# Kernel tuning notes

Hardware: AMD Instinct MI355X
Metric: run time of the kernel (lower is better)

The kernel has to match this reference:

```python
import jax, jax.numpy as jnp
import numpy as np

N_NODES = 10000
N_EDGES = 640000
D_FEAT = 128


def setup_inputs() -> dict:
    key = jax.random.key(0)
    k1, k2, k3 = jax.random.split(key, 3)
    node_feats = jax.random.normal(k1, (N_NODES, D_FEAT), dtype=jnp.float32)
    src = jax.random.randint(k2, (N_EDGES,), 0, N_NODES, dtype=jnp.int64)
    dst = jax.random.randint(k3, (N_EDGES,), 0, N_NODES, dtype=jnp.int64)
    return {"node_feats": node_feats, "src": src, "dst": dst}


def reference(node_feats, src, dst):
    # copy_u: message on each edge is the source node's feature -> [E, D]
    # max reduce: per-destination segment max -> [N, D]
    messages = node_feats[src]
    h_max = jax.ops.segment_max(messages, dst, num_segments=N_NODES)
    # DGL fills nodes with zero in-degree with 0 for max reduce; segment_max
    # yields -inf for empty segments, so replace those with 0.
    in_deg = jax.ops.segment_sum(
        jnp.ones((dst.shape[0],), dtype=jnp.int32), dst, num_segments=N_NODES
    )
    h_max = jnp.where((in_deg > 0)[:, None], h_max, jnp.zeros((), node_feats.dtype))
    return h_max
```

## Files before the change

kernel.cpp:

```cpp
#include <hip/hip_runtime.h>
#include <math.h>

#define NBINS   10000
#define NB      256
#define PSTRIDE 10016
#define HWORDS  5008
#define PAD     160

__device__ __forceinline__ unsigned short f2bf(float x) {
    unsigned int u = __float_as_uint(x);
    unsigned int r = (u + 0x7fffu + ((u >> 16) & 1u)) >> 16;
    return (unsigned short)r;
}
__device__ __forceinline__ float bf2f(unsigned short b) {
    return __uint_as_float(((unsigned int)b) << 16);
}

__global__ __launch_bounds__(256) void hist_convert_kernel(
        const int* __restrict__ dst, const float* __restrict__ feats,
        unsigned short* __restrict__ partial, unsigned short* __restrict__ feats_bf,
        int E, int chunk, int nf4) {
    const float4* f4 = (const float4*)feats;
    ushort4* b4 = (ushort4*)feats_bf;
    for (int i = blockIdx.x * blockDim.x + threadIdx.x; i < nf4;
         i += gridDim.x * blockDim.x) {
        float4 v = f4[i];
        ushort4 o;
        o.x = f2bf(v.x); o.y = f2bf(v.y); o.z = f2bf(v.z); o.w = f2bf(v.w);
        b4[i] = o;
    }
    __shared__ unsigned int h[HWORDS];
    for (int i = threadIdx.x; i < HWORDS; i += 256) h[i] = 0u;
    __syncthreads();
    int b = blockIdx.x;
    int start = b * chunk;
    int end   = min(start + chunk, E);
    for (int e = start + threadIdx.x; e < end; e += 256) {
        int d = dst[e];
        atomicAdd(&h[d >> 1], 1u << ((d & 1) * 16));
    }
    __syncthreads();
    unsigned int* row = (unsigned int*)(partial + (size_t)b * PSTRIDE);
    for (int i = threadIdx.x; i < HWORDS; i += 256) row[i] = h[i];
}

__global__ __launch_bounds__(256) void colscan_kernel(unsigned short* __restrict__ partial,
                                                      int* __restrict__ deg, int nbins) {
    int bin = blockIdx.x * blockDim.x + threadIdx.x;
    if (bin >= nbins) return;
    int running = 0;
    for (int b = 0; b < NB; b += 16) {
        int v[16];
        #pragma unroll
        for (int k = 0; k < 16; k++)
            v[k] = partial[(size_t)(b + k) * PSTRIDE + bin];
        #pragma unroll
        for (int k = 0; k < 16; k++) {
            partial[(size_t)(b + k) * PSTRIDE + bin] = (unsigned short)running;
            running += v[k];
        }
    }
    deg[bin] = running;
}

__global__ __launch_bounds__(256) void scatter_kernel(const int* __restrict__ src,
                                                      const int* __restrict__ dst,
                                                      const unsigned short* __restrict__ partial,
                                                      unsigned short* __restrict__ edge_pad,
                                                      int E, int chunk) {
    __shared__ unsigned int h[HWORDS];
    for (int i = threadIdx.x; i < HWORDS; i += 256) h[i] = 0u;
    __syncthreads();
    int b = blockIdx.x;
    const unsigned short* base = partial + (size_t)b * PSTRIDE;
    int start = b * chunk;
    int end   = min(start + chunk, E);
    for (int e = start + threadIdx.x; e < end; e += 256) {
        int d = dst[e];
        unsigned int old = atomicAdd(&h[d >> 1], 1u << ((d & 1) * 16));
        int r = (int)((old >> ((d & 1) * 16)) & 0xffffu);
        edge_pad[(size_t)d * PAD + (int)base[d] + r] = (unsigned short)src[e];
    }
}

__global__ __launch_bounds__(256) void gather_max_kernel(
        const unsigned short* __restrict__ feats_bf, const int* __restrict__ deg,
        const unsigned short* __restrict__ edge_pad, float* __restrict__ out,
        int n_nodes) {
    int gtid    = blockIdx.x * blockDim.x + threadIdx.x;
    int wave_id = gtid >> 6;
    int lane    = threadIdx.x & 63;
    int half    = lane >> 5;
    int col     = lane & 31;
    int node    = wave_id * 2 + half;
    if (node >= n_nodes) return;

    int dg = deg[node];
    const unsigned short* ep = edge_pad + (size_t)node * PAD;
    const ushort4* f4 = (const ushort4*)feats_bf;
    float4 acc = make_float4(-INFINITY, -INFINITY, -INFINITY, -INFINITY);

    int j = 0;
    for (; j + 8 <= dg; j += 8) {
        uint4 w = *(const uint4*)(ep + j);
        int e0 = w.x & 0xffff, e1 = w.x >> 16;
        int e2 = w.y & 0xffff, e3 = w.y >> 16;
        int e4 = w.z & 0xffff, e5 = w.z >> 16;
        int e6 = w.w & 0xffff, e7 = w.w >> 16;
        ushort4 v0 = f4[(size_t)e0 * 32 + col];
        ushort4 v1 = f4[(size_t)e1 * 32 + col];
        ushort4 v2 = f4[(size_t)e2 * 32 + col];
        ushort4 v3 = f4[(size_t)e3 * 32 + col];
        ushort4 v4 = f4[(size_t)e4 * 32 + col];
        ushort4 v5 = f4[(size_t)e5 * 32 + col];
        ushort4 v6 = f4[(size_t)e6 * 32 + col];
        ushort4 v7 = f4[(size_t)e7 * 32 + col];
        acc.x = fmaxf(acc.x, fmaxf(fmaxf(fmaxf(bf2f(v0.x), bf2f(v1.x)), fmaxf(bf2f(v2.x), bf2f(v3.x))),
                                   fmaxf(fmaxf(bf2f(v4.x), bf2f(v5.x)), fmaxf(bf2f(v6.x), bf2f(v7.x)))));
        acc.y = fmaxf(acc.y, fmaxf(fmaxf(fmaxf(bf2f(v0.y), bf2f(v1.y)), fmaxf(bf2f(v2.y), bf2f(v3.y))),
                                   fmaxf(fmaxf(bf2f(v4.y), bf2f(v5.y)), fmaxf(bf2f(v6.y), bf2f(v7.y)))));
        acc.z = fmaxf(acc.z, fmaxf(fmaxf(fmaxf(bf2f(v0.z), bf2f(v1.z)), fmaxf(bf2f(v2.z), bf2f(v3.z))),
                                   fmaxf(fmaxf(bf2f(v4.z), bf2f(v5.z)), fmaxf(bf2f(v6.z), bf2f(v7.z)))));
        acc.w = fmaxf(acc.w, fmaxf(fmaxf(fmaxf(bf2f(v0.w), bf2f(v1.w)), fmaxf(bf2f(v2.w), bf2f(v3.w))),
                                   fmaxf(fmaxf(bf2f(v4.w), bf2f(v5.w)), fmaxf(bf2f(v6.w), bf2f(v7.w)))));
    }
    for (; j < dg; ++j) {
        int e0 = ep[j];
        ushort4 v = f4[(size_t)e0 * 32 + col];
        acc.x = fmaxf(acc.x, bf2f(v.x));
        acc.y = fmaxf(acc.y, bf2f(v.y));
        acc.z = fmaxf(acc.z, bf2f(v.z));
        acc.w = fmaxf(acc.w, bf2f(v.w));
    }

    if (dg == 0) { acc.x = 0.f; acc.y = 0.f; acc.z = 0.f; acc.w = 0.f; }
    ((float4*)out)[(size_t)node * 32 + col] = acc;
}

extern "C" void kernel_launch(void* const* d_in, const int* in_sizes, int n_in,
                              void* d_out, int out_size, void* d_ws, size_t ws_size,
                              hipStream_t stream) {
    const float* feats = (const float*)d_in[0];
    const int*   src   = (const int*)d_in[1];
    const int*   dst   = (const int*)d_in[2];
    float*       out   = (float*)d_out;

    const int E = in_sizes[1];
    const int N = NBINS;
    const int chunk = (E + NB - 1) / NB;
    const int nf4   = (N * 128) / 4;

    char* w = (char*)d_ws;
    unsigned short* partial = (unsigned short*)w;
    w += (size_t)NB * PSTRIDE * sizeof(unsigned short);
    int* deg = (int*)w;  w += (size_t)PSTRIDE * sizeof(int);
    unsigned short* edge_pad = (unsigned short*)w;
    w += (size_t)N * PAD * sizeof(unsigned short);
    unsigned short* feats_bf = (unsigned short*)w;

    hist_convert_kernel<<<NB, 256, 0, stream>>>(dst, feats, partial, feats_bf, E, chunk, nf4);
    colscan_kernel<<<(N + 255) / 256, 256, 0, stream>>>(partial, deg, N);
    scatter_kernel<<<NB, 256, 0, stream>>>(src, dst, partial, edge_pad, E, chunk);

    int waves    = (N + 1) / 2;
    int threads  = waves * 64;
    int blocks_g = (threads + 255) / 256;
    gather_max_kernel<<<blocks_g, 256, 0, stream>>>(feats_bf, deg, edge_pad, out, N);
}
```

Measured before the change: 107.1 us.

## Fuse histogram, scan and scatter into one per-chunk local counting-sort kernel

Replaces the three-kernel global CSR build (per-block histograms, column scan, padded scatter) with a single kernel. Sixteen blocks each sort a 40000-edge chunk locally in shared memory and write per-node offsets into a small transposed table. The gather kernel then walks 16 segments per node instead of one contiguous padded list. This saves launches and the large partial-histogram traffic, but the gather now does more scattered index loads and serial per-segment loops, and only 16 blocks do the sort.

```diff
diff --git a/kernel.cpp b/kernel.cpp
--- a/kernel.cpp
+++ b/kernel.cpp
@@ -2,10 +2,10 @@
 #include <math.h>
 
 #define NBINS   10000
-#define NB      256
-#define PSTRIDE 10016
+#define NBS     16
+#define CHUNK   40000
 #define HWORDS  5008
-#define PAD     160
+#define TROW    16
 
 __device__ __forceinline__ unsigned short f2bf(float x) {
     unsigned int u = __float_as_uint(x);
@@ -16,77 +16,90 @@
     return __uint_as_float(((unsigned int)b) << 16);
 }
 
-__global__ __launch_bounds__(256) void hist_convert_kernel(
-        const int* __restrict__ dst, const float* __restrict__ feats,
-        unsigned short* __restrict__ partial, unsigned short* __restrict__ feats_bf,
-        int E, int chunk, int nf4) {
-    const float4* f4 = (const float4*)feats;
-    ushort4* b4 = (ushort4*)feats_bf;
-    for (int i = blockIdx.x * blockDim.x + threadIdx.x; i < nf4;
-         i += gridDim.x * blockDim.x) {
-        float4 v = f4[i];
-        ushort4 o;
-        o.x = f2bf(v.x); o.y = f2bf(v.y); o.z = f2bf(v.z); o.w = f2bf(v.w);
-        b4[i] = o;
+__global__ __launch_bounds__(256) void build_kernel(
+        const int* __restrict__ dst, const int* __restrict__ src,
+        const float* __restrict__ feats, unsigned short* __restrict__ trans,
+        unsigned short* __restrict__ edge_sorted, unsigned short* __restrict__ feats_bf,
+        int E, int nf4) {
+    {
+        const float4* f4 = (const float4*)feats;
+        ushort4* b4 = (ushort4*)feats_bf;
+        for (int i = blockIdx.x * blockDim.x + threadIdx.x; i < nf4;
+             i += gridDim.x * blockDim.x) {
+            float4 v = f4[i];
+            ushort4 o;
+            o.x = f2bf(v.x); o.y = f2bf(v.y); o.z = f2bf(v.z); o.w = f2bf(v.w);
+            b4[i] = o;
+        }
     }
+    if (blockIdx.x >= NBS) return;
+
     __shared__ unsigned int h[HWORDS];
-    for (int i = threadIdx.x; i < HWORDS; i += 256) h[i] = 0u;
+    __shared__ int wsums[4];
+    const int b   = blockIdx.x;
+    const int tid = threadIdx.x;
+    const int lane = tid & 63;
+    const int wave = tid >> 6;
+    const int start = b * CHUNK;
+    const int end   = min(start + CHUNK, E);
+
+    for (int i = tid; i < HWORDS; i += 256) h[i] = 0u;
     __syncthreads();
-    int b = blockIdx.x;
-    int start = b * chunk;
-    int end   = min(start + chunk, E);
-    for (int e = start + threadIdx.x; e < end; e += 256) {
+    for (int e = start + tid; e < end; e += 256) {
         int d = dst[e];
         atomicAdd(&h[d >> 1], 1u << ((d & 1) * 16));
     }
     __syncthreads();
-    unsigned int* row = (unsigned int*)(partial + (size_t)b * PSTRIDE);
-    for (int i = threadIdx.x; i < HWORDS; i += 256) row[i] = h[i];
-}
 
-__global__ __launch_bounds__(256) void colscan_kernel(unsigned short* __restrict__ partial,
-                                                      int* __restrict__ deg, int nbins) {
-    int bin = blockIdx.x * blockDim.x + threadIdx.x;
-    if (bin >= nbins) return;
-    int running = 0;
-    for (int b = 0; b < NB; b += 16) {
-        int v[16];
-        #pragma unroll
-        for (int k = 0; k < 16; k++)
-            v[k] = partial[(size_t)(b + k) * PSTRIDE + bin];
-        #pragma unroll
-        for (int k = 0; k < 16; k++) {
-            partial[(size_t)(b + k) * PSTRIDE + bin] = (unsigned short)running;
-            running += v[k];
-        }
+    int w0 = tid * 20;
+    int w1 = min(w0 + 20, HWORDS);
+    int s = 0;
+    for (int w = w0; w < w1; ++w) {
+        unsigned int u = h[w];
+        s += (int)(u & 0xffffu) + (int)(u >> 16);
     }
-    deg[bin] = running;
-}
+    int incl = s;
+    #pragma unroll
+    for (int off = 1; off < 64; off <<= 1) {
+        int t = __shfl_up(incl, off, 64);
+        if (lane >= off) incl += t;
+    }
+    if (lane == 63) wsums[wave] = incl;
+    __syncthreads();
+    int wpre = 0;
+    #pragma unroll
+    for (int k = 0; k < 4; k++) if (k < wave) wpre += wsums[k];
+    int running = wpre + incl - s;
+    for (int w = w0; w < w1; ++w) {
+        unsigned int u = h[w];
+        int c0 = (int)(u & 0xffffu);
+        int c1 = (int)(u >> 16);
+        h[w] = (unsigned int)running | ((unsigned int)(running + c0) << 16);
+        running += c0 + c1;
+    }
+    __syncthreads();
 
-__global__ __launch_bounds__(256) void scatter_kernel(const int* __restrict__ src,
-                                                      const int* __restrict__ dst,
-                                                      const unsigned short* __restrict__ partial,
-                                                      unsigned short* __restrict__ edge_pad,
-                                                      int E, int chunk) {
-    __shared__ unsigned int h[HWORDS];
-    for (int i = threadIdx.x; i < HWORDS; i += 256) h[i] = 0u;
+    for (int i = tid; i < NBINS; i += 256) {
+        unsigned int u = h[i >> 1];
+        trans[(size_t)i * TROW + b] = (unsigned short)((u >> ((i & 1) * 16)) & 0xffffu);
+    }
+    if (tid == 0) trans[(size_t)NBINS * TROW + b] = (unsigned short)max(0, end - start);
     __syncthreads();
-    int b = blockIdx.x;
-    const unsigned short* base = partial + (size_t)b * PSTRIDE;
-    int start = b * chunk;
-    int end   = min(start + chunk, E);
-    for (int e = start + threadIdx.x; e < end; e += 256) {
+
+    unsigned short* reg = edge_sorted + (size_t)b * CHUNK;
+    for (int e = start + tid; e < end; e += 256) {
         int d = dst[e];
         unsigned int old = atomicAdd(&h[d >> 1], 1u << ((d & 1) * 16));
-        int r = (int)((old >> ((d & 1) * 16)) & 0xffffu);
-        edge_pad[(size_t)d * PAD + (int)base[d] + r] = (unsigned short)src[e];
+        int pos = (int)((old >> ((d & 1) * 16)) & 0xffffu);
+        reg[pos] = (unsigned short)src[e];
     }
 }
 
 __global__ __launch_bounds__(256) void gather_max_kernel(
-        const unsigned short* __restrict__ feats_bf, const int* __restrict__ deg,
-        const unsigned short* __restrict__ edge_pad, float* __restrict__ out,
-        int n_nodes) {
+        const unsigned short* __restrict__ feats_bf,
+        const unsigned short* __restrict__ trans,
+        const unsigned short* __restrict__ edge_sorted,
+        float* __restrict__ out, int n_nodes) {
     int gtid    = blockIdx.x * blockDim.x + threadIdx.x;
     int wave_id = gtid >> 6;
     int lane    = threadIdx.x & 63;
@@ -95,45 +108,45 @@
     int node    = wave_id * 2 + half;
     if (node >= n_nodes) return;
 
-    int dg = deg[node];
-    const unsigned short* ep = edge_pad + (size_t)node * PAD;
+    const uint4* tp = (const uint4*)trans;
+    union { uint4 v[2]; unsigned short s[16]; } O0, O1;
+    O0.v[0] = tp[(size_t)node * 2];
+    O0.v[1] = tp[(size_t)node * 2 + 1];
+    O1.v[0] = tp[(size_t)(node + 1) * 2];
+    O1.v[1] = tp[(size_t)(node + 1) * 2 + 1];
+
     const ushort4* f4 = (const ushort4*)feats_bf;
     float4 acc = make_float4(-INFINITY, -INFINITY, -INFINITY, -INFINITY);
+    int deg = 0;
 
-    int j = 0;
-    for (; j + 8 <= dg; j += 8) {
-        uint4 w = *(const uint4*)(ep + j);
-        int e0 = w.x & 0xffff, e1 = w.x >> 16;
-        int e2 = w.y & 0xffff, e3 = w.y >> 16;
-        int e4 = w.z & 0xffff, e5 = w.z >> 16;
-        int e6 = w.w & 0xffff, e7 = w.w >> 16;
-        ushort4 v0 = f4[(size_t)e0 * 32 + col];
-        ushort4 v1 = f4[(size_t)e1 * 32 + col];
-        ushort4 v2 = f4[(size_t)e2 * 32 + col];
-        ushort4 v3 = f4[(size_t)e3 * 32 + col];
-        ushort4 v4 = f4[(size_t)e4 * 32 + col];
-        ushort4 v5 = f4[(size_t)e5 * 32 + col];
-        ushort4 v6 = f4[(size_t)e6 * 32 + col];
-        ushort4 v7 = f4[(size_t)e7 * 32 + col];
-        acc.x = fmaxf(acc.x, fmaxf(fmaxf(fmaxf(bf2f(v0.x), bf2f(v1.x)), fmaxf(bf2f(v2.x), bf2f(v3.x))),
-                                   fmaxf(fmaxf(bf2f(v4.x), bf2f(v5.x)), fmaxf(bf2f(v6.x), bf2f(v7.x)))));
-        acc.y = fmaxf(acc.y, fmaxf(fmaxf(fmaxf(bf2f(v0.y), bf2f(v1.y)), fmaxf(bf2f(v2.y), bf2f(v3.y))),
-                                   fmaxf(fmaxf(bf2f(v4.y), bf2f(v5.y)), fmaxf(bf2f(v6.y), bf2f(v7.y)))));
-        acc.z = fmaxf(acc.z, fmaxf(fmaxf(fmaxf(bf2f(v0.z), bf2f(v1.z)), fmaxf(bf2f(v2.z), bf2f(v3.z))),
-                                   fmaxf(fmaxf(bf2f(v4.z), bf2f(v5.z)), fmaxf(bf2f(v6.z), bf2f(v7.z)))));
-        acc.w = fmaxf(acc.w, fmaxf(fmaxf(fmaxf(bf2f(v0.w), bf2f(v1.w)), fmaxf(bf2f(v2.w), bf2f(v3.w))),
-                                   fmaxf(fmaxf(bf2f(v4.w), bf2f(v5.w)), fmaxf(bf2f(v6.w), bf2f(v7.w)))));
-    }
-    for (; j < dg; ++j) {
-        int e0 = ep[j];
-        ushort4 v = f4[(size_t)e0 * 32 + col];
-        acc.x = fmaxf(acc.x, bf2f(v.x));
-        acc.y = fmaxf(acc.y, bf2f(v.y));
-        acc.z = fmaxf(acc.z, bf2f(v.z));
-        acc.w = fmaxf(acc.w, bf2f(v.w));
+    #pragma unroll
+    for (int b = 0; b < NBS; b++) {
+        int j0 = O0.s[b];
+        int j1 = O1.s[b];
+        deg += j1 - j0;
+        const unsigned short* ep = edge_sorted + (size_t)b * CHUNK;
+        int j = j0;
+        for (; j + 2 <= j1; j += 2) {
+            int e0 = ep[j];
+            int e1 = ep[j + 1];
+            ushort4 v0 = f4[(size_t)e0 * 32 + col];
+            ushort4 v1 = f4[(size_t)e1 * 32 + col];
+            acc.x = fmaxf(acc.x, fmaxf(bf2f(v0.x), bf2f(v1.x)));
+            acc.y = fmaxf(acc.y, fmaxf(bf2f(v0.y), bf2f(v1.y)));
+            acc.z = fmaxf(acc.z, fmaxf(bf2f(v0.z), bf2f(v1.z)));
+            acc.w = fmaxf(acc.w, fmaxf(bf2f(v0.w), bf2f(v1.w)));
+        }
+        if (j < j1) {
+            int e0 = ep[j];
+            ushort4 v = f4[(size_t)e0 * 32 + col];
+            acc.x = fmaxf(acc.x, bf2f(v.x));
+            acc.y = fmaxf(acc.y, bf2f(v.y));
+            acc.z = fmaxf(acc.z, bf2f(v.z));
+            acc.w = fmaxf(acc.w, bf2f(v.w));
+        }
     }
 
-    if (dg == 0) { acc.x = 0.f; acc.y = 0.f; acc.z = 0.f; acc.w = 0.f; }
+    if (deg == 0) { acc.x = 0.f; acc.y = 0.f; acc.z = 0.f; acc.w = 0.f; }
     ((float4*)out)[(size_t)node * 32 + col] = acc;
 }
 
@@ -145,25 +158,22 @@
     const int*   dst   = (const int*)d_in[2];
     float*       out   = (float*)d_out;
 
-    const int E = in_sizes[1];
-    const int N = NBINS;
-    const int chunk = (E + NB - 1) / NB;
-    const int nf4   = (N * 128) / 4;
+    const int E   = in_sizes[1];
+    const int N   = NBINS;
+    const int nf4 = (N * 128) / 4;
 
     char* w = (char*)d_ws;
-    unsigned short* partial = (unsigned short*)w;
-    w += (size_t)NB * PSTRIDE * sizeof(unsigned short);
-    int* deg = (int*)w;  w += (size_t)PSTRIDE * sizeof(int);
-    unsigned short* edge_pad = (unsigned short*)w;
-    w += (size_t)N * PAD * sizeof(unsigned short);
+    unsigned short* trans = (unsigned short*)w;
+    w += ((size_t)(N + 1) * TROW * sizeof(unsigned short) + 63) & ~(size_t)63;
+    unsigned short* edge_sorted = (unsigned short*)w;
+    w += ((size_t)NBS * CHUNK * sizeof(unsigned short) + 63) & ~(size_t)63;
     unsigned short* feats_bf = (unsigned short*)w;
 
-    hist_convert_kernel<<<NB, 256, 0, stream>>>(dst, feats, partial, feats_bf, E, chunk, nf4);
-    colscan_kernel<<<(N + 255) / 256, 256, 0, stream>>>(partial, deg, N);
-    scatter_kernel<<<NB, 256, 0, stream>>>(src, dst, partial, edge_pad, E, chunk);
+    build_kernel<<<256, 256, 0, stream>>>(dst, src, feats, trans, edge_sorted,
+                                          feats_bf, E, nf4);
 
     int waves    = (N + 1) / 2;
     int threads  = waves * 64;
     int blocks_g = (threads + 255) / 256;
-    gather_max_kernel<<<blocks_g, 256, 0, stream>>>(feats_bf, deg, edge_pad, out, N);
+    gather_max_kernel<<<blocks_g, 256, 0, stream>>>(feats_bf, trans, edge_sorted, out, N);
 }
```

After: 211.3 us. 1.97x slower.
